# Performance work log

Hardware: AMD Instinct MI355X
Metric: run time of the kernel (lower is better)

Reference implementation:

```python
import jax, jax.numpy as jnp
import numpy as np

E = 1024
B, QL, KVL = 8, 2048, 2048


def setup_inputs() -> dict:
    key = jax.random.key(0)
    ks = jax.random.split(key, 12)
    s = 1.0 / np.sqrt(E)
    return {
        "query": jax.random.normal(ks[0], (B, QL, E), jnp.float32),
        "key_value": jax.random.normal(ks[1], (B, KVL, E), jnp.float32),
        "attention_mask": jax.random.randint(ks[2], (B, QL, KVL), 0, 2, jnp.int32),
        "Wq": jax.random.uniform(ks[3], (E, E), jnp.float32, -s, s),
        "bq": jax.random.uniform(ks[4], (E,), jnp.float32, -s, s),
        "Wk": jax.random.uniform(ks[5], (E, E), jnp.float32, -s, s),
        "bk": jax.random.uniform(ks[6], (E,), jnp.float32, -s, s),
        "Wv": jax.random.uniform(ks[7], (E, E), jnp.float32, -s, s),
        "bv": jax.random.uniform(ks[8], (E,), jnp.float32, -s, s),
        "Wo": jax.random.uniform(ks[9], (E, E), jnp.float32, -s, s),
        "bo": jax.random.uniform(ks[10], (E,), jnp.float32, -s, s),
    }


def reference(query, key_value, attention_mask, Wq, bq, Wk, bk, Wv, bv, Wo, bo):
    # torch Linear: x @ W.T + b
    q = jnp.einsum('bqe,fe->bqf', query, Wq) + bq          # [B, QL, E]
    k = jnp.einsum('bke,fe->bkf', key_value, Wk) + bk      # [B, KVL, E]
    v = jnp.einsum('bke,fe->bkf', key_value, Wv) + bv      # [B, KVL, E]
    scale = 1.0 / jnp.sqrt(jnp.asarray(q.shape[-1], q.dtype))
    attn = jnp.einsum('bqe,bke->bqk', q, k) * scale        # [B, QL, KVL]
    attn = jnp.where(attention_mask == 0, -jnp.inf, attn)
    attn = jax.nn.softmax(attn, axis=-1)
    out = jnp.einsum('bqk,bke->bqe', attn, v)              # [B, QL, E]
    out = jnp.einsum('bqe,fe->bqf', out, Wo) + bo
    return out
```

## Files before the change

kernel.cpp:

```cpp
#include <hip/hip_runtime.h>
#include <hip/hip_bf16.h>
#include <stdint.h>

typedef unsigned short u16;
typedef short s16x8 __attribute__((ext_vector_type(8)));
typedef u16 u16x8 __attribute__((ext_vector_type(8)));
typedef u16 u16x4 __attribute__((ext_vector_type(4)));
typedef float f32x4 __attribute__((ext_vector_type(4)));

__device__ __forceinline__ u16 f2bf(float f) {
  union { float f; uint32_t u; } c; c.f = f;
  uint32_t u = c.u;
  u = u + 0x7fffu + ((u >> 16) & 1u);
  return (u16)(u >> 16);
}
__device__ __forceinline__ float bf2f(u16 b) {
  union { uint32_t u; float f; } c; c.u = ((uint32_t)b) << 16;
  return c.f;
}

__device__ __forceinline__ void gld_lds16(const u16* g, u16* l) {
  __builtin_amdgcn_global_load_lds(
      (const __attribute__((address_space(1))) uint32_t*)g,
      (__attribute__((address_space(3))) uint32_t*)l,
      16, 0, 0);
}

__global__ __launch_bounds__(256) void cvt_f32_to_bf16(
    const float* __restrict__ in, u16* __restrict__ out, long n8) {
  long i = (long)blockIdx.x * blockDim.x + threadIdx.x;
  if (i >= n8) return;
  const float4 a = ((const float4*)in)[i * 2];
  const float4 b = ((const float4*)in)[i * 2 + 1];
  u16x8 r;
  r[0] = f2bf(a.x); r[1] = f2bf(a.y); r[2] = f2bf(a.z); r[3] = f2bf(a.w);
  r[4] = f2bf(b.x); r[5] = f2bf(b.y); r[6] = f2bf(b.z); r[7] = f2bf(b.w);
  *(u16x8*)&out[i * 8] = r;
}

__global__ __launch_bounds__(256) void cvt_w4(
    const float* __restrict__ w0, const float* __restrict__ w1,
    const float* __restrict__ w2, const float* __restrict__ w3,
    u16* __restrict__ out) {
  const float* src = (blockIdx.y == 0) ? w0 : (blockIdx.y == 1) ? w1
                   : (blockIdx.y == 2) ? w2 : w3;
  const long i = (long)blockIdx.x * blockDim.x + threadIdx.x;
  const float4 a = ((const float4*)src)[i * 2];
  const float4 b = ((const float4*)src)[i * 2 + 1];
  u16x8 r;
  r[0] = f2bf(a.x); r[1] = f2bf(a.y); r[2] = f2bf(a.z); r[3] = f2bf(a.w);
  r[4] = f2bf(b.x); r[5] = f2bf(b.y); r[6] = f2bf(b.z); r[7] = f2bf(b.w);
  *(u16x8*)&out[(long)blockIdx.y * 1048576 + i * 8] = r;
}

__global__ __launch_bounds__(256) void softmax_mask_rows(
    u16* __restrict__ S, const int* __restrict__ mask) {
  const long base = (long)blockIdx.x * 2048;
  const int tid = threadIdx.x;
  const int lane = tid & 63, wave = tid >> 6;
  u16x8 raw = *(const u16x8*)&S[base + tid * 8];
  const int4 m0 = ((const int4*)(mask + base))[tid * 2];
  const int4 m1 = ((const int4*)(mask + base))[tid * 2 + 1];
  float v[8];
  v[0] = m0.x ? bf2f(raw[0]) : -1e30f;
  v[1] = m0.y ? bf2f(raw[1]) : -1e30f;
  v[2] = m0.z ? bf2f(raw[2]) : -1e30f;
  v[3] = m0.w ? bf2f(raw[3]) : -1e30f;
  v[4] = m1.x ? bf2f(raw[4]) : -1e30f;
  v[5] = m1.y ? bf2f(raw[5]) : -1e30f;
  v[6] = m1.z ? bf2f(raw[6]) : -1e30f;
  v[7] = m1.w ? bf2f(raw[7]) : -1e30f;
  float m = v[0];
#pragma unroll
  for (int j = 1; j < 8; ++j) m = fmaxf(m, v[j]);
#pragma unroll
  for (int off = 32; off >= 1; off >>= 1) m = fmaxf(m, __shfl_xor(m, off));
  __shared__ float red[8];
  if (lane == 0) red[wave] = m;
  __syncthreads();
  m = fmaxf(fmaxf(red[0], red[1]), fmaxf(red[2], red[3]));
  float s = 0.f;
#pragma unroll
  for (int j = 0; j < 8; ++j) { v[j] = __expf(v[j] - m); s += v[j]; }
#pragma unroll
  for (int off = 32; off >= 1; off >>= 1) s += __shfl_xor(s, off);
  if (lane == 0) red[4 + wave] = s;
  __syncthreads();
  s = (red[4] + red[5]) + (red[6] + red[7]);
  const float inv = 1.f / s;
#pragma unroll
  for (int j = 0; j < 8; ++j) raw[j] = f2bf(v[j] * inv);
  *(u16x8*)&S[base + tid * 8] = raw;
}

union __align__(16) SmemT {
  u16 stage[2][128 * 64];
  float epi[64 * 132];
};

__device__ __forceinline__ s16x8 ldsfrag(const u16* p, int r, int c8) {
  return *(const s16x8*)&p[r * 64 + ((c8 ^ (r & 7)) << 3)];
}

__device__ __forceinline__ void stage128(const u16* __restrict__ gb, int row0,
                                         int K, int k0, u16* lbuf, int tid) {
#pragma unroll
  for (int i = 0; i < 4; ++i) {
    const int f = i * 256 + tid;
    const int rl = f >> 3, s = f & 7;
    const int gc = (s ^ (rl & 7)) << 3;
    gld_lds16(gb + (long)(row0 + rl) * K + k0 + gc, lbuf + f * 8);
  }
}

template<bool HAS_BIAS, int MODE>
__global__ __launch_bounds__(256, 4) void gemm128(
    const u16* __restrict__ A, const u16* __restrict__ B,
    const float* __restrict__ bias, const float* __restrict__ bias2,
    void* __restrict__ Cv, void* __restrict__ Cv2,
    int M, int N, int K, long sA, long sB, long sC, float scale) {
  __shared__ SmemT sm;
  const int nx = gridDim.x, ny = gridDim.y;
  const int did = blockIdx.x + nx * (blockIdx.y + ny * blockIdx.z);
  const int cpx = (nx * ny * gridDim.z) >> 3;
  const int nf = (did & 7) * cpx + (did >> 3);
  const int b = nf / (nx * ny);
  const int rr = nf % (nx * ny);
  const int bm = (rr / ny) * 128;
  const int bn = (rr % ny) * 128;

  const u16* Ab = A + (long)b * sA;
  const u16* Bb = B + (long)b * sB;
  const int tid = threadIdx.x;
  const int lane = tid & 63, wave = tid >> 6;
  const int wm = wave >> 1, wn = wave & 1;
  const int lr = lane & 15, lk = lane >> 4;
  const int NT = K >> 6;

  f32x4 acc[4][4] = {};

  for (int t = 0; t < NT; ++t) {
    stage128(Ab, bm, K, t << 6, sm.stage[0], tid);
    stage128(Bb, bn, K, t << 6, sm.stage[1], tid);
    asm volatile("s_waitcnt vmcnt(0)" ::: "memory");
    __syncthreads();
#pragma unroll
    for (int ks = 0; ks < 2; ++ks) {
      s16x8 af[4], bg[4];
#pragma unroll
      for (int mi = 0; mi < 4; ++mi)
        af[mi] = ldsfrag(sm.stage[0], wm * 64 + mi * 16 + lr, ks * 4 + lk);
#pragma unroll
      for (int ni = 0; ni < 4; ++ni)
        bg[ni] = ldsfrag(sm.stage[1], wn * 64 + ni * 16 + lr, ks * 4 + lk);
#pragma unroll
      for (int mi = 0; mi < 4; ++mi)
#pragma unroll
        for (int ni = 0; ni < 4; ++ni)
          acc[mi][ni] = __builtin_amdgcn_mfma_f32_16x16x32_bf16(
              af[mi], bg[ni], acc[mi][ni], 0, 0, 0);
    }
    __syncthreads();
  }

  const long cb = (long)b * sC;
  if (MODE == 2 && bn >= 1024) {
#pragma unroll
    for (int mi = 0; mi < 4; ++mi) {
#pragma unroll
      for (int ni = 0; ni < 4; ++ni) {
        const int row0 = bm + wm * 64 + mi * 16 + (lk << 2);
        const int col2 = (bn - 1024) + wn * 64 + ni * 16 + lr;
        const float bvx = HAS_BIAS ? bias2[col2] : 0.f;
        u16x4 pk;
#pragma unroll
        for (int j = 0; j < 4; ++j) pk[j] = f2bf(acc[mi][ni][j] * scale + bvx);
        const long ad = (long)(row0 >> 11) * (2048L * 1024) +
                        (long)col2 * 2048 + (row0 & 2047);
        *(u16x4*)&((u16*)Cv2)[ad] = pk;
      }
    }
  } else {
    const int ldC = (MODE == 2) ? 1024 : N;
    const int q = tid & 3, r = tid >> 2;
#pragma unroll
    for (int h = 0; h < 2; ++h) {
      __syncthreads();
      if (wm == h) {
#pragma unroll
        for (int mi = 0; mi < 4; ++mi)
#pragma unroll
          for (int ni = 0; ni < 4; ++ni) {
            const int c = wn * 64 + ni * 16 + lr;
            const float bvx = HAS_BIAS ? bias[bn + c] : 0.f;
#pragma unroll
            for (int j = 0; j < 4; ++j)
              sm.epi[(mi * 16 + (lk << 2) + j) * 132 + c] =
                  acc[mi][ni][j] * scale + bvx;
          }
      }
      __syncthreads();
      const long grow = cb + (long)(bm + h * 64 + r) * ldC + bn;
#pragma unroll
      for (int ch = 0; ch < 4; ++ch) {
        const int c0 = q * 8 + ch * 32;
        const float4 x = *(const float4*)&sm.epi[r * 132 + c0];
        const float4 y = *(const float4*)&sm.epi[r * 132 + c0 + 4];
        if (MODE == 1) {
          *(float4*)&((float*)Cv)[grow + c0] = x;
          *(float4*)&((float*)Cv)[grow + c0 + 4] = y;
        } else {
          u16x8 pk;
          pk[0] = f2bf(x.x); pk[1] = f2bf(x.y);
          pk[2] = f2bf(x.z); pk[3] = f2bf(x.w);
          pk[4] = f2bf(y.x); pk[5] = f2bf(y.y);
          pk[6] = f2bf(y.z); pk[7] = f2bf(y.w);
          *(u16x8*)&((u16*)Cv)[grow + c0] = pk;
        }
      }
    }
  }
}

extern "C" void kernel_launch(void* const* d_in, const int* in_sizes, int n_in,
                              void* d_out, int out_size, void* d_ws, size_t ws_size,
                              hipStream_t stream) {
  const float* query = (const float*)d_in[0];
  const float* kv    = (const float*)d_in[1];
  const int*   mask  = (const int*)d_in[2];
  const float* Wq = (const float*)d_in[3];
  const float* bq = (const float*)d_in[4];
  const float* Wk = (const float*)d_in[5];
  const float* bk = (const float*)d_in[6];
  const float* Wv = (const float*)d_in[7];
  const float* bv = (const float*)d_in[8];
  const float* Wo = (const float*)d_in[9];
  const float* bo = (const float*)d_in[10];
  float* out = (float*)d_out;

  char* ws = (char*)d_ws;
  const size_t MB = (size_t)1 << 20;
  u16* qbf  = (u16*)(ws + 0);
  u16* kvbf = (u16*)(ws + 32 * MB);
  u16* wq   = (u16*)(ws + 64 * MB);
  u16* wk   = (u16*)(ws + 66 * MB);
  u16* wo   = (u16*)(ws + 70 * MB);
  u16* Q    = (u16*)(ws + 72 * MB);
  u16* Kb   = (u16*)(ws + 104 * MB);
  u16* Vt   = (u16*)(ws + 136 * MB);
  u16* S    = (u16*)(ws + 168 * MB);
  u16* O    = qbf;

  const long sQK = (long)2048 * 1024;
  const long sS  = (long)2048 * 2048;

  cvt_f32_to_bf16<<<8192, 256, 0, stream>>>(query, qbf, 2097152);
  cvt_f32_to_bf16<<<8192, 256, 0, stream>>>(kv, kvbf, 2097152);
  cvt_w4<<<dim3(512, 4, 1), 256, 0, stream>>>(Wq, Wk, Wv, Wo, wq);

  gemm128<true, 0><<<dim3(128, 8, 1), 256, 0, stream>>>(
      qbf, wq, bq, nullptr, Q, nullptr, 16384, 1024, 1024, 0, 0, 0, 1.f);

  gemm128<true, 2><<<dim3(128, 16, 1), 256, 0, stream>>>(
      kvbf, wk, bk, bv, Kb, Vt, 16384, 2048, 1024, 0, 0, 0, 1.f);

  gemm128<false, 0><<<dim3(16, 16, 8), 256, 0, stream>>>(
      Q, Kb, nullptr, nullptr, S, nullptr, 2048, 2048, 1024, sQK, sQK, sS, 0.03125f);

  softmax_mask_rows<<<16384, 256, 0, stream>>>(S, mask);

  gemm128<false, 0><<<dim3(16, 8, 8), 256, 0, stream>>>(
      S, Vt, nullptr, nullptr, O, nullptr, 2048, 1024, 2048, sS, sQK, sQK, 1.f);

  gemm128<true, 1><<<dim3(128, 8, 1), 256, 0, stream>>>(
      O, wo, bo, nullptr, out, nullptr, 16384, 1024, 1024, 0, 0, 0, 1.f);
}
```

Baseline: 381.0 us.

## Fuse attention mask into QK^T GEMM epilogue and shrink epilogue LDS

```diff
diff --git a/kernel.cpp b/kernel.cpp
--- a/kernel.cpp
+++ b/kernel.cpp
@@ -53,23 +53,14 @@
   *(u16x8*)&out[(long)blockIdx.y * 1048576 + i * 8] = r;
 }
 
-__global__ __launch_bounds__(256) void softmax_mask_rows(
-    u16* __restrict__ S, const int* __restrict__ mask) {
+__global__ __launch_bounds__(256) void softmax_rows(u16* __restrict__ S) {
   const long base = (long)blockIdx.x * 2048;
   const int tid = threadIdx.x;
   const int lane = tid & 63, wave = tid >> 6;
   u16x8 raw = *(const u16x8*)&S[base + tid * 8];
-  const int4 m0 = ((const int4*)(mask + base))[tid * 2];
-  const int4 m1 = ((const int4*)(mask + base))[tid * 2 + 1];
   float v[8];
-  v[0] = m0.x ? bf2f(raw[0]) : -1e30f;
-  v[1] = m0.y ? bf2f(raw[1]) : -1e30f;
-  v[2] = m0.z ? bf2f(raw[2]) : -1e30f;
-  v[3] = m0.w ? bf2f(raw[3]) : -1e30f;
-  v[4] = m1.x ? bf2f(raw[4]) : -1e30f;
-  v[5] = m1.y ? bf2f(raw[5]) : -1e30f;
-  v[6] = m1.z ? bf2f(raw[6]) : -1e30f;
-  v[7] = m1.w ? bf2f(raw[7]) : -1e30f;
+#pragma unroll
+  for (int j = 0; j < 8; ++j) v[j] = bf2f(raw[j]);
   float m = v[0];
 #pragma unroll
   for (int j = 1; j < 8; ++j) m = fmaxf(m, v[j]);
@@ -95,7 +86,7 @@
 
 union __align__(16) SmemT {
   u16 stage[2][128 * 64];
-  float epi[64 * 132];
+  float epi[32 * 132];
 };
 
 __device__ __forceinline__ s16x8 ldsfrag(const u16* p, int r, int c8) {
@@ -113,12 +104,13 @@
   }
 }
 
-template<bool HAS_BIAS, int MODE>
-__global__ __launch_bounds__(256, 4) void gemm128(
+template<bool HAS_BIAS, int MODE, bool HAS_MASK>
+__global__ __launch_bounds__(256, 5) void gemm128(
     const u16* __restrict__ A, const u16* __restrict__ B,
     const float* __restrict__ bias, const float* __restrict__ bias2,
-    void* __restrict__ Cv, void* __restrict__ Cv2,
-    int M, int N, int K, long sA, long sB, long sC, float scale) {
+    const int* __restrict__ mask, void* __restrict__ Cv,
+    void* __restrict__ Cv2,
+    int M, int N, int K, long sA, long sB, long sC, long sMask, float scale) {
   __shared__ SmemT sm;
   const int nx = gridDim.x, ny = gridDim.y;
   const int did = blockIdx.x + nx * (blockIdx.y + ny * blockIdx.z);
@@ -182,28 +174,34 @@
     }
   } else {
     const int ldC = (MODE == 2) ? 1024 : N;
-    const int q = tid & 3, r = tid >> 2;
-#pragma unroll
-    for (int h = 0; h < 2; ++h) {
+    const int q = tid & 7, r = tid >> 3;
+#pragma unroll
+    for (int h = 0; h < 4; ++h) {
       __syncthreads();
-      if (wm == h) {
-#pragma unroll
-        for (int mi = 0; mi < 4; ++mi)
+      if (wm == (h >> 1)) {
+        const int mi0 = (h & 1) * 2;
+#pragma unroll
+        for (int mm = 0; mm < 2; ++mm) {
+          const int mi = mi0 + mm;
 #pragma unroll
           for (int ni = 0; ni < 4; ++ni) {
             const int c = wn * 64 + ni * 16 + lr;
             const float bvx = HAS_BIAS ? bias[bn + c] : 0.f;
 #pragma unroll
             for (int j = 0; j < 4; ++j)
-              sm.epi[(mi * 16 + (lk << 2) + j) * 132 + c] =
+              sm.epi[(mm * 16 + (lk << 2) + j) * 132 + c] =
                   acc[mi][ni][j] * scale + bvx;
           }
+        }
       }
       __syncthreads();
-      const long grow = cb + (long)(bm + h * 64 + r) * ldC + bn;
-#pragma unroll
-      for (int ch = 0; ch < 4; ++ch) {
-        const int c0 = q * 8 + ch * 32;
+      const int growi = bm + h * 32 + r;
+      const long grow = cb + (long)growi * ldC + bn;
+      const long mrow = HAS_MASK
+          ? ((long)b * sMask + (long)growi * (long)N + bn) : 0;
+#pragma unroll
+      for (int ch = 0; ch < 2; ++ch) {
+        const int c0 = ch * 64 + q * 8;
         const float4 x = *(const float4*)&sm.epi[r * 132 + c0];
         const float4 y = *(const float4*)&sm.epi[r * 132 + c0 + 4];
         if (MODE == 1) {
@@ -211,10 +209,23 @@
           *(float4*)&((float*)Cv)[grow + c0 + 4] = y;
         } else {
           u16x8 pk;
-          pk[0] = f2bf(x.x); pk[1] = f2bf(x.y);
-          pk[2] = f2bf(x.z); pk[3] = f2bf(x.w);
-          pk[4] = f2bf(y.x); pk[5] = f2bf(y.y);
-          pk[6] = f2bf(y.z); pk[7] = f2bf(y.w);
+          if (HAS_MASK) {
+            const int4 ma = *(const int4*)&mask[mrow + c0];
+            const int4 mb = *(const int4*)&mask[mrow + c0 + 4];
+            pk[0] = f2bf(ma.x ? x.x : -1e30f);
+            pk[1] = f2bf(ma.y ? x.y : -1e30f);
+            pk[2] = f2bf(ma.z ? x.z : -1e30f);
+            pk[3] = f2bf(ma.w ? x.w : -1e30f);
+            pk[4] = f2bf(mb.x ? y.x : -1e30f);
+            pk[5] = f2bf(mb.y ? y.y : -1e30f);
+            pk[6] = f2bf(mb.z ? y.z : -1e30f);
+            pk[7] = f2bf(mb.w ? y.w : -1e30f);
+          } else {
+            pk[0] = f2bf(x.x); pk[1] = f2bf(x.y);
+            pk[2] = f2bf(x.z); pk[3] = f2bf(x.w);
+            pk[4] = f2bf(y.x); pk[5] = f2bf(y.y);
+            pk[6] = f2bf(y.z); pk[7] = f2bf(y.w);
+          }
           *(u16x8*)&((u16*)Cv)[grow + c0] = pk;
         }
       }
@@ -258,20 +269,25 @@
   cvt_f32_to_bf16<<<8192, 256, 0, stream>>>(kv, kvbf, 2097152);
   cvt_w4<<<dim3(512, 4, 1), 256, 0, stream>>>(Wq, Wk, Wv, Wo, wq);
 
-  gemm128<true, 0><<<dim3(128, 8, 1), 256, 0, stream>>>(
-      qbf, wq, bq, nullptr, Q, nullptr, 16384, 1024, 1024, 0, 0, 0, 1.f);
-
-  gemm128<true, 2><<<dim3(128, 16, 1), 256, 0, stream>>>(
-      kvbf, wk, bk, bv, Kb, Vt, 16384, 2048, 1024, 0, 0, 0, 1.f);
-
-  gemm128<false, 0><<<dim3(16, 16, 8), 256, 0, stream>>>(
-      Q, Kb, nullptr, nullptr, S, nullptr, 2048, 2048, 1024, sQK, sQK, sS, 0.03125f);
-
-  softmax_mask_rows<<<16384, 256, 0, stream>>>(S, mask);
-
-  gemm128<false, 0><<<dim3(16, 8, 8), 256, 0, stream>>>(
-      S, Vt, nullptr, nullptr, O, nullptr, 2048, 1024, 2048, sS, sQK, sQK, 1.f);
-
-  gemm128<true, 1><<<dim3(128, 8, 1), 256, 0, stream>>>(
-      O, wo, bo, nullptr, out, nullptr, 16384, 1024, 1024, 0, 0, 0, 1.f);
-}
+  gemm128<true, 0, false><<<dim3(128, 8, 1), 256, 0, stream>>>(
+      qbf, wq, bq, nullptr, nullptr, Q, nullptr,
+      16384, 1024, 1024, 0, 0, 0, 0, 1.f);
+
+  gemm128<true, 2, false><<<dim3(128, 16, 1), 256, 0, stream>>>(
+      kvbf, wk, bk, bv, nullptr, Kb, Vt,
+      16384, 2048, 1024, 0, 0, 0, 0, 1.f);
+
+  gemm128<false, 0, true><<<dim3(16, 16, 8), 256, 0, stream>>>(
+      Q, Kb, nullptr, nullptr, mask, S, nullptr,
+      2048, 2048, 1024, sQK, sQK, sS, sS, 0.03125f);
+
+  softmax_rows<<<16384, 256, 0, stream>>>(S);
+
+  gemm128<false, 0, false><<<dim3(16, 8, 8), 256, 0, stream>>>(
+      S, Vt, nullptr, nullptr, nullptr, O, nullptr,
+      2048, 1024, 2048, sS, sQK, sQK, 0, 1.f);
+
+  gemm128<true, 1, false><<<dim3(128, 8, 1), 256, 0, stream>>>(
+      O, wo, bo, nullptr, nullptr, out, nullptr,
+      16384, 1024, 1024, 0, 0, 0, 0, 1.f);
+}
```

Result: slower. 585.4 us (+53.7%).
